# Optimization experiments

Measured on AMD Instinct MI355X. Metric: run time of the kernel, lower is better.

Reference implementation:

```python
import jax, jax.numpy as jnp
import numpy as np

WS = 11  # window_size
PAD = WS // 2
C1 = 0.01 ** 2
C2 = 0.03 ** 2

def _gaussian_window(ws=WS, sigma=1.5):
    # NOTE: original create_window hardcodes sigma=1.5 regardless of init arg
    x = np.arange(ws, dtype=np.float64)
    g = np.exp(-(x - ws // 2) ** 2 / (2.0 * sigma ** 2))
    g = g / g.sum()
    w = np.outer(g, g).astype(np.float32)
    return jnp.asarray(w)[None, None, :, :]  # [1,1,ws,ws] (OIHW)

def _conv(x, k):
    # x: [B,1,H,W], k: [1,1,ws,ws], SAME padding via explicit pad
    return jax.lax.conv_general_dilated(
        x, k, window_strides=(1, 1), padding=[(PAD, PAD), (PAD, PAD)],
        dimension_numbers=('NCHW', 'OIHW', 'NCHW'))

def setup_inputs() -> dict:
    key = jax.random.key(0)
    k1, k2 = jax.random.split(key)
    B, H, W = 32, 768, 768
    pred = jax.random.uniform(k1, (B, 1, H, W), dtype=jnp.float32)
    y = jax.random.uniform(k2, (B, 1, H, W), dtype=jnp.float32)
    return {"pred": pred, "y": y}

def reference(pred, y):
    k = _gaussian_window()
    mu1 = _conv(pred, k)
    mu2 = _conv(y, k)
    mu1_sq = mu1 * mu1
    mu2_sq = mu2 * mu2
    mu1_mu2 = mu1 * mu2
    sigma1_sq = _conv(pred * pred, k) - mu1_sq
    sigma2_sq = _conv(y * y, k) - mu2_sq
    sigma12 = _conv(pred * y, k) - mu1_mu2
    luminance = (2.0 * mu1_mu2 + C1) / (mu1_sq + mu2_sq + C1)
    contrast = (2.0 * sigma12 + C2) / (sigma1_sq + sigma2_sq + C2)
    structure = (sigma12 + C2 / 2.0) / (jnp.sqrt(sigma1_sq * sigma2_sq) + C2 / 2.0)
    ssim_map = luminance * contrast * structure  # [B,1,H,W]
    per_sample = jnp.mean(ssim_map, axis=(1, 2, 3))  # mean per sample, as in the loop
    return jnp.mean(per_sample)
```

## Files before the change

### kernel.cpp

```cpp
#include <hip/hip_runtime.h>

#define TW 32
#define TH 32
#define SH 42
#define HPITCH 36
#define BLOCK 256
#define IMG_W 768
#define IMG_H 768
#define IMG_B 32
#define GX_ (IMG_W / TW)
#define GY_ (IMG_H / TH)
#define NBLOCKS (GX_ * GY_ * IMG_B)

#define W0 0.00102838f
#define W1 0.00759876f
#define W2 0.03600077f
#define W3 0.10936069f
#define W4 0.21300554f
#define W5 0.26601173f

__global__ __launch_bounds__(BLOCK, 5) void ssim_tile_kernel(
    const float* __restrict__ pred, const float* __restrict__ yin,
    float* __restrict__ partial)
{
    constexpr float GW[11] = {W0, W1, W2, W3, W4, W5, W4, W3, W2, W1, W0};

    __shared__ __align__(16) float Hb[5][SH][HPITCH];
    __shared__ float wsum[BLOCK / 64];

    const int tid = threadIdx.x;
    const int x0 = blockIdx.x * TW;
    const int y0 = blockIdx.y * TH;
    const size_t base = (size_t)blockIdx.z * (size_t)(IMG_H * IMG_W);
    const float* pb = pred + base;
    const float* yb = yin + base;

    const bool interior = (x0 >= 8) && (x0 + TW + 8 <= IMG_W) &&
                          (y0 >= 5) && (y0 + TH + 5 <= IMG_H);

    for (int it = tid; it < SH * 8; it += BLOCK) {
        const int hr = it >> 3;
        const int c0 = (it & 7) << 2;
        const int gy = y0 + hr - 5;
        float p[14], q[14];

        if (interior) {
            const float* rp = pb + (size_t)gy * IMG_W + (x0 + c0 - 8);
            const float* rq = yb + (size_t)gy * IMG_W + (x0 + c0 - 8);
            p[0] = rp[3];
            *(float4*)(p + 1) = *(const float4*)(rp + 4);
            *(float4*)(p + 5) = *(const float4*)(rp + 8);
            *(float4*)(p + 9) = *(const float4*)(rp + 12);
            p[13] = rp[16];
            q[0] = rq[3];
            *(float4*)(q + 1) = *(const float4*)(rq + 4);
            *(float4*)(q + 5) = *(const float4*)(rq + 8);
            *(float4*)(q + 9) = *(const float4*)(rq + 12);
            q[13] = rq[16];
        } else {
            if (gy >= 0 && gy < IMG_H) {
                const float* rowp = pb + (size_t)gy * IMG_W;
                const float* rowq = yb + (size_t)gy * IMG_W;
                #pragma unroll
                for (int k = 0; k < 14; ++k) {
                    const int gx = x0 + c0 - 5 + k;
                    const bool in = (gx >= 0) && (gx < IMG_W);
                    p[k] = in ? rowp[gx] : 0.f;
                    q[k] = in ? rowq[gx] : 0.f;
                }
            } else {
                #pragma unroll
                for (int k = 0; k < 14; ++k) { p[k] = 0.f; q[k] = 0.f; }
            }
        }

        {
            float a0 = 0.f, a1 = 0.f, a2 = 0.f, a3 = 0.f;
            #pragma unroll
            for (int t = 0; t < 11; ++t) {
                const float w = GW[t];
                a0 += w * p[t]; a1 += w * p[t + 1];
                a2 += w * p[t + 2]; a3 += w * p[t + 3];
            }
            *(float4*)&Hb[0][hr][c0] = make_float4(a0, a1, a2, a3);
        }
        {
            float a0 = 0.f, a1 = 0.f, a2 = 0.f, a3 = 0.f;
            #pragma unroll
            for (int t = 0; t < 11; ++t) {
                const float w = GW[t];
                a0 += w * q[t]; a1 += w * q[t + 1];
                a2 += w * q[t + 2]; a3 += w * q[t + 3];
            }
            *(float4*)&Hb[1][hr][c0] = make_float4(a0, a1, a2, a3);
        }
        {
            float t14[14];
            #pragma unroll
            for (int k = 0; k < 14; ++k) t14[k] = p[k] * p[k];
            float a0 = 0.f, a1 = 0.f, a2 = 0.f, a3 = 0.f;
            #pragma unroll
            for (int t = 0; t < 11; ++t) {
                const float w = GW[t];
                a0 += w * t14[t]; a1 += w * t14[t + 1];
                a2 += w * t14[t + 2]; a3 += w * t14[t + 3];
            }
            *(float4*)&Hb[2][hr][c0] = make_float4(a0, a1, a2, a3);
        }
        {
            float t14[14];
            #pragma unroll
            for (int k = 0; k < 14; ++k) t14[k] = q[k] * q[k];
            float a0 = 0.f, a1 = 0.f, a2 = 0.f, a3 = 0.f;
            #pragma unroll
            for (int t = 0; t < 11; ++t) {
                const float w = GW[t];
                a0 += w * t14[t]; a1 += w * t14[t + 1];
                a2 += w * t14[t + 2]; a3 += w * t14[t + 3];
            }
            *(float4*)&Hb[3][hr][c0] = make_float4(a0, a1, a2, a3);
        }
        {
            float t14[14];
            #pragma unroll
            for (int k = 0; k < 14; ++k) t14[k] = p[k] * q[k];
            float a0 = 0.f, a1 = 0.f, a2 = 0.f, a3 = 0.f;
            #pragma unroll
            for (int t = 0; t < 11; ++t) {
                const float w = GW[t];
                a0 += w * t14[t]; a1 += w * t14[t + 1];
                a2 += w * t14[t + 2]; a3 += w * t14[t + 3];
            }
            *(float4*)&Hb[4][hr][c0] = make_float4(a0, a1, a2, a3);
        }
    }
    __syncthreads();

    const int vc  = tid & 31;
    const int vr0 = (tid >> 5) << 2;
    float acc[5][4];
    #pragma unroll
    for (int ch = 0; ch < 5; ++ch) {
        const float* hb = &Hb[ch][vr0][vc];
        float v[14];
        #pragma unroll
        for (int j = 0; j < 14; ++j) v[j] = hb[j * HPITCH];
        #pragma unroll
        for (int o = 0; o < 4; ++o) {
            float a = 0.f;
            #pragma unroll
            for (int t = 0; t < 11; ++t)
                a += GW[t] * v[o + t];
            acc[ch][o] = a;
        }
    }

    const float C1f = 1e-4f;
    const float C2f = 9e-4f;
    float lsum = 0.f;
    #pragma unroll
    for (int o = 0; o < 4; ++o) {
        float mu1 = acc[0][o], mu2 = acc[1][o];
        float m11 = acc[2][o], m22 = acc[3][o], m12 = acc[4][o];
        float mu1s = mu1 * mu1;
        float mu2s = mu2 * mu2;
        float mu12 = mu1 * mu2;
        float s1  = m11 - mu1s;
        float s2  = m22 - mu2s;
        float s12 = m12 - mu12;
        float num = (2.f * mu12 + C1f) * (2.f * s12 + C2f) * (s12 + 0.5f * C2f);
        float den = (mu1s + mu2s + C1f) * (s1 + s2 + C2f) * (sqrtf(s1 * s2) + 0.5f * C2f);
        lsum += num / den;
    }

    #pragma unroll
    for (int off = 32; off > 0; off >>= 1)
        lsum += __shfl_xor(lsum, off);
    const int wid  = tid >> 6;
    const int lane = tid & 63;
    if (lane == 0) wsum[wid] = lsum;
    __syncthreads();
    if (tid == 0) {
        const int bid = (blockIdx.z * GY_ + blockIdx.y) * GX_ + blockIdx.x;
        partial[bid] = wsum[0] + wsum[1] + wsum[2] + wsum[3];
    }
}

__global__ __launch_bounds__(1024) void ssim_reduce_kernel(
    const float* __restrict__ partial, float* __restrict__ out)
{
    __shared__ double sd[1024];
    double s = 0.0;
    const float4* p4 = (const float4*)partial;
    for (int i = threadIdx.x; i < NBLOCKS / 4; i += 1024) {
        float4 v = p4[i];
        s += (double)v.x + (double)v.y + (double)v.z + (double)v.w;
    }
    sd[threadIdx.x] = s;
    __syncthreads();
    #pragma unroll
    for (int st = 512; st > 0; st >>= 1) {
        if (threadIdx.x < st) sd[threadIdx.x] += sd[threadIdx.x + st];
        __syncthreads();
    }
    if (threadIdx.x == 0)
        out[0] = (float)(sd[0] * (1.0 / ((double)IMG_B * IMG_H * IMG_W)));
}

extern "C" void kernel_launch(void* const* d_in, const int* in_sizes, int n_in,
                              void* d_out, int out_size, void* d_ws, size_t ws_size,
                              hipStream_t stream)
{
    const float* pred = (const float*)d_in[0];
    const float* yin  = (const float*)d_in[1];
    float* out     = (float*)d_out;
    float* partial = (float*)d_ws;

    dim3 grid(GX_, GY_, IMG_B);
    ssim_tile_kernel<<<grid, BLOCK, 0, stream>>>(pred, yin, partial);
    ssim_reduce_kernel<<<1, 1024, 0, stream>>>(partial, out);
}
```

Before: 247.8 us.

## Split SSIM tile into two passes to shrink shared memory and raise occupancy

Splits the separable convolution into two passes. The first pass computes and vertically reduces the means using a two-channel buffer. The second pass reloads the inputs and computes the three second-moment channels in a three-channel shared buffer. This cuts shared memory per block from five channels to three, so launch bounds can rise from 5 to 8 blocks per CU. The cost is loading the input tile twice and an extra barrier. The change also swaps sqrtf and the division for hardware approximate sqrt and reciprocal, which may slightly change precision.

```diff
diff --git a/kernel.cpp b/kernel.cpp
--- a/kernel.cpp
+++ b/kernel.cpp
@@ -19,13 +19,26 @@
 #define W4 0.21300554f
 #define W5 0.26601173f
 
-__global__ __launch_bounds__(BLOCK, 5) void ssim_tile_kernel(
+__device__ __forceinline__ void hconv14(const float x[14], float* dst)
+{
+    constexpr float GW[11] = {W0, W1, W2, W3, W4, W5, W4, W3, W2, W1, W0};
+    float a0 = 0.f, a1 = 0.f, a2 = 0.f, a3 = 0.f;
+    #pragma unroll
+    for (int t = 0; t < 11; ++t) {
+        const float w = GW[t];
+        a0 += w * x[t];     a1 += w * x[t + 1];
+        a2 += w * x[t + 2]; a3 += w * x[t + 3];
+    }
+    *(float4*)dst = make_float4(a0, a1, a2, a3);
+}
+
+__global__ __launch_bounds__(BLOCK, 8) void ssim_tile_kernel(
     const float* __restrict__ pred, const float* __restrict__ yin,
     float* __restrict__ partial)
 {
     constexpr float GW[11] = {W0, W1, W2, W3, W4, W5, W4, W3, W2, W1, W0};
 
-    __shared__ __align__(16) float Hb[5][SH][HPITCH];
+    __shared__ __align__(16) float Hb[3][SH][HPITCH];
     __shared__ float wsum[BLOCK / 64];
 
     const int tid = threadIdx.x;
@@ -37,6 +50,9 @@
 
     const bool interior = (x0 >= 8) && (x0 + TW + 8 <= IMG_W) &&
                           (y0 >= 5) && (y0 + TH + 5 <= IMG_H);
+
+    const int vc  = tid & 31;
+    const int vr0 = (tid >> 5) << 2;
 
     for (int it = tid; it < SH * 8; it += BLOCK) {
         const int hr = it >> 3;
@@ -73,85 +89,102 @@
                 for (int k = 0; k < 14; ++k) { p[k] = 0.f; q[k] = 0.f; }
             }
         }
-
-        {
-            float a0 = 0.f, a1 = 0.f, a2 = 0.f, a3 = 0.f;
-            #pragma unroll
-            for (int t = 0; t < 11; ++t) {
-                const float w = GW[t];
-                a0 += w * p[t]; a1 += w * p[t + 1];
-                a2 += w * p[t + 2]; a3 += w * p[t + 3];
-            }
-            *(float4*)&Hb[0][hr][c0] = make_float4(a0, a1, a2, a3);
-        }
-        {
-            float a0 = 0.f, a1 = 0.f, a2 = 0.f, a3 = 0.f;
-            #pragma unroll
-            for (int t = 0; t < 11; ++t) {
-                const float w = GW[t];
-                a0 += w * q[t]; a1 += w * q[t + 1];
-                a2 += w * q[t + 2]; a3 += w * q[t + 3];
-            }
-            *(float4*)&Hb[1][hr][c0] = make_float4(a0, a1, a2, a3);
-        }
-        {
-            float t14[14];
-            #pragma unroll
-            for (int k = 0; k < 14; ++k) t14[k] = p[k] * p[k];
-            float a0 = 0.f, a1 = 0.f, a2 = 0.f, a3 = 0.f;
-            #pragma unroll
-            for (int t = 0; t < 11; ++t) {
-                const float w = GW[t];
-                a0 += w * t14[t]; a1 += w * t14[t + 1];
-                a2 += w * t14[t + 2]; a3 += w * t14[t + 3];
-            }
-            *(float4*)&Hb[2][hr][c0] = make_float4(a0, a1, a2, a3);
-        }
-        {
-            float t14[14];
-            #pragma unroll
-            for (int k = 0; k < 14; ++k) t14[k] = q[k] * q[k];
-            float a0 = 0.f, a1 = 0.f, a2 = 0.f, a3 = 0.f;
-            #pragma unroll
-            for (int t = 0; t < 11; ++t) {
-                const float w = GW[t];
-                a0 += w * t14[t]; a1 += w * t14[t + 1];
-                a2 += w * t14[t + 2]; a3 += w * t14[t + 3];
-            }
-            *(float4*)&Hb[3][hr][c0] = make_float4(a0, a1, a2, a3);
-        }
-        {
-            float t14[14];
-            #pragma unroll
-            for (int k = 0; k < 14; ++k) t14[k] = p[k] * q[k];
-            float a0 = 0.f, a1 = 0.f, a2 = 0.f, a3 = 0.f;
-            #pragma unroll
-            for (int t = 0; t < 11; ++t) {
-                const float w = GW[t];
-                a0 += w * t14[t]; a1 += w * t14[t + 1];
-                a2 += w * t14[t + 2]; a3 += w * t14[t + 3];
-            }
-            *(float4*)&Hb[4][hr][c0] = make_float4(a0, a1, a2, a3);
-        }
-    }
-    __syncthreads();
-
-    const int vc  = tid & 31;
-    const int vr0 = (tid >> 5) << 2;
-    float acc[5][4];
-    #pragma unroll
-    for (int ch = 0; ch < 5; ++ch) {
-        const float* hb = &Hb[ch][vr0][vc];
+        hconv14(p, &Hb[0][hr][c0]);
+        hconv14(q, &Hb[1][hr][c0]);
+    }
+    __syncthreads();
+
+    float mu1v[4], mu2v[4];
+    {
         float v[14];
-        #pragma unroll
-        for (int j = 0; j < 14; ++j) v[j] = hb[j * HPITCH];
+        const float* hb0 = &Hb[0][vr0][vc];
+        #pragma unroll
+        for (int j = 0; j < 14; ++j) v[j] = hb0[j * HPITCH];
         #pragma unroll
         for (int o = 0; o < 4; ++o) {
             float a = 0.f;
             #pragma unroll
-            for (int t = 0; t < 11; ++t)
-                a += GW[t] * v[o + t];
-            acc[ch][o] = a;
+            for (int t = 0; t < 11; ++t) a += GW[t] * v[o + t];
+            mu1v[o] = a;
+        }
+        const float* hb1 = &Hb[1][vr0][vc];
+        #pragma unroll
+        for (int j = 0; j < 14; ++j) v[j] = hb1[j * HPITCH];
+        #pragma unroll
+        for (int o = 0; o < 4; ++o) {
+            float a = 0.f;
+            #pragma unroll
+            for (int t = 0; t < 11; ++t) a += GW[t] * v[o + t];
+            mu2v[o] = a;
+        }
+    }
+    __syncthreads();
+
+    for (int it = tid; it < SH * 8; it += BLOCK) {
+        const int hr = it >> 3;
+        const int c0 = (it & 7) << 2;
+        const int gy = y0 + hr - 5;
+        float p[14], q[14];
+
+        if (interior) {
+            const float* rp = pb + (size_t)gy * IMG_W + (x0 + c0 - 8);
+            const float* rq = yb + (size_t)gy * IMG_W + (x0 + c0 - 8);
+            p[0] = rp[3];
+            *(float4*)(p + 1) = *(const float4*)(rp + 4);
+            *(float4*)(p + 5) = *(const float4*)(rp + 8);
+            *(float4*)(p + 9) = *(const float4*)(rp + 12);
+            p[13] = rp[16];
+            q[0] = rq[3];
+            *(float4*)(q + 1) = *(const float4*)(rq + 4);
+            *(float4*)(q + 5) = *(const float4*)(rq + 8);
+            *(float4*)(q + 9) = *(const float4*)(rq + 12);
+            q[13] = rq[16];
+        } else {
+            if (gy >= 0 && gy < IMG_H) {
+                const float* rowp = pb + (size_t)gy * IMG_W;
+                const float* rowq = yb + (size_t)gy * IMG_W;
+                #pragma unroll
+                for (int k = 0; k < 14; ++k) {
+                    const int gx = x0 + c0 - 5 + k;
+                    const bool in = (gx >= 0) && (gx < IMG_W);
+                    p[k] = in ? rowp[gx] : 0.f;
+                    q[k] = in ? rowq[gx] : 0.f;
+                }
+            } else {
+                #pragma unroll
+                for (int k = 0; k < 14; ++k) { p[k] = 0.f; q[k] = 0.f; }
+            }
+        }
+        float t14[14];
+        #pragma unroll
+        for (int k = 0; k < 14; ++k) t14[k] = p[k] * p[k];
+        hconv14(t14, &Hb[0][hr][c0]);
+        #pragma unroll
+        for (int k = 0; k < 14; ++k) t14[k] = q[k] * q[k];
+        hconv14(t14, &Hb[1][hr][c0]);
+        #pragma unroll
+        for (int k = 0; k < 14; ++k) t14[k] = p[k] * q[k];
+        hconv14(t14, &Hb[2][hr][c0]);
+    }
+    __syncthreads();
+
+    float m11v[4], m22v[4], m12v[4];
+    {
+        float v[14];
+        #pragma unroll
+        for (int ch = 0; ch < 3; ++ch) {
+            const float* hb = &Hb[ch][vr0][vc];
+            #pragma unroll
+            for (int j = 0; j < 14; ++j) v[j] = hb[j * HPITCH];
+            #pragma unroll
+            for (int o = 0; o < 4; ++o) {
+                float a = 0.f;
+                #pragma unroll
+                for (int t = 0; t < 11; ++t) a += GW[t] * v[o + t];
+                if (ch == 0) m11v[o] = a;
+                else if (ch == 1) m22v[o] = a;
+                else m12v[o] = a;
+            }
         }
     }
 
@@ -160,17 +193,17 @@
     float lsum = 0.f;
     #pragma unroll
     for (int o = 0; o < 4; ++o) {
-        float mu1 = acc[0][o], mu2 = acc[1][o];
-        float m11 = acc[2][o], m22 = acc[3][o], m12 = acc[4][o];
+        float mu1 = mu1v[o], mu2 = mu2v[o];
         float mu1s = mu1 * mu1;
         float mu2s = mu2 * mu2;
         float mu12 = mu1 * mu2;
-        float s1  = m11 - mu1s;
-        float s2  = m22 - mu2s;
-        float s12 = m12 - mu12;
+        float s1  = m11v[o] - mu1s;
+        float s2  = m22v[o] - mu2s;
+        float s12 = m12v[o] - mu12;
         float num = (2.f * mu12 + C1f) * (2.f * s12 + C2f) * (s12 + 0.5f * C2f);
-        float den = (mu1s + mu2s + C1f) * (s1 + s2 + C2f) * (sqrtf(s1 * s2) + 0.5f * C2f);
-        lsum += num / den;
+        float den = (mu1s + mu2s + C1f) * (s1 + s2 + C2f) *
+                    (__builtin_amdgcn_sqrtf(s1 * s2) + 0.5f * C2f);
+        lsum += num * __builtin_amdgcn_rcpf(den);
     }
 
     #pragma unroll
```

Result: slower. 464.9 us (+87.6%).

## Pack pred/y channel pairs into float2 to use packed FMA for Gaussian blur

Applied to the files above, without the earlier changes.

Interleaves the pred and y values (and their squares) into two-wide vectors so both horizontal and vertical 11-tap passes can use packed fp32 math (v_pk_fma) on paired channels. Shared memory is reorganized into two float2 planes plus one scalar plane for pred*y. The final SSIM division and sqrt are replaced with hardware approximate rcp and sqrt intrinsics. This aims to halve the FMA instruction count in the compute-bound blur, at the cost of slightly lower precision and possible LDS bank pattern changes from 8-byte elements.

```diff
diff --git a/kernel.cpp b/kernel.cpp
--- a/kernel.cpp
+++ b/kernel.cpp
@@ -1,8 +1,11 @@
 #include <hip/hip_runtime.h>
+
+typedef float f32x2 __attribute__((ext_vector_type(2)));
 
 #define TW 32
 #define TH 32
 #define SH 42
+#define PITCH2 34
 #define HPITCH 36
 #define BLOCK 256
 #define IMG_W 768
@@ -19,13 +22,17 @@
 #define W4 0.21300554f
 #define W5 0.26601173f
 
+__device__ __forceinline__ f32x2 sp2(float s) { f32x2 v; v.x = s; v.y = s; return v; }
+
 __global__ __launch_bounds__(BLOCK, 5) void ssim_tile_kernel(
     const float* __restrict__ pred, const float* __restrict__ yin,
     float* __restrict__ partial)
 {
     constexpr float GW[11] = {W0, W1, W2, W3, W4, W5, W4, W3, W2, W1, W0};
 
-    __shared__ __align__(16) float Hb[5][SH][HPITCH];
+    __shared__ __align__(16) f32x2 Hmu[SH][PITCH2];
+    __shared__ __align__(16) f32x2 Hsq[SH][PITCH2];
+    __shared__ __align__(16) float Hpq[SH][HPITCH];
     __shared__ float wsum[BLOCK / 64];
 
     const int tid = threadIdx.x;
@@ -74,85 +81,95 @@
             }
         }
 
+        f32x2 d[14];
+        #pragma unroll
+        for (int k = 0; k < 14; ++k) { f32x2 t; t.x = p[k]; t.y = q[k]; d[k] = t; }
+
+        {
+            f32x2 a0 = sp2(0.f), a1 = sp2(0.f), a2 = sp2(0.f), a3 = sp2(0.f);
+            #pragma unroll
+            for (int k = 0; k < 14; ++k) {
+                const f32x2 v = d[k];
+                if (k <= 10)           a0 += sp2(GW[k])     * v;
+                if (k >= 1 && k <= 11) a1 += sp2(GW[k - 1]) * v;
+                if (k >= 2 && k <= 12) a2 += sp2(GW[k - 2]) * v;
+                if (k >= 3)            a3 += sp2(GW[k - 3]) * v;
+            }
+            Hmu[hr][c0]     = a0;
+            Hmu[hr][c0 + 1] = a1;
+            Hmu[hr][c0 + 2] = a2;
+            Hmu[hr][c0 + 3] = a3;
+        }
+        {
+            f32x2 a0 = sp2(0.f), a1 = sp2(0.f), a2 = sp2(0.f), a3 = sp2(0.f);
+            #pragma unroll
+            for (int k = 0; k < 14; ++k) {
+                const f32x2 v = d[k] * d[k];
+                if (k <= 10)           a0 += sp2(GW[k])     * v;
+                if (k >= 1 && k <= 11) a1 += sp2(GW[k - 1]) * v;
+                if (k >= 2 && k <= 12) a2 += sp2(GW[k - 2]) * v;
+                if (k >= 3)            a3 += sp2(GW[k - 3]) * v;
+            }
+            Hsq[hr][c0]     = a0;
+            Hsq[hr][c0 + 1] = a1;
+            Hsq[hr][c0 + 2] = a2;
+            Hsq[hr][c0 + 3] = a3;
+        }
         {
             float a0 = 0.f, a1 = 0.f, a2 = 0.f, a3 = 0.f;
             #pragma unroll
-            for (int t = 0; t < 11; ++t) {
-                const float w = GW[t];
-                a0 += w * p[t]; a1 += w * p[t + 1];
-                a2 += w * p[t + 2]; a3 += w * p[t + 3];
-            }
-            *(float4*)&Hb[0][hr][c0] = make_float4(a0, a1, a2, a3);
-        }
-        {
-            float a0 = 0.f, a1 = 0.f, a2 = 0.f, a3 = 0.f;
-            #pragma unroll
-            for (int t = 0; t < 11; ++t) {
-                const float w = GW[t];
-                a0 += w * q[t]; a1 += w * q[t + 1];
-                a2 += w * q[t + 2]; a3 += w * q[t + 3];
-            }
-            *(float4*)&Hb[1][hr][c0] = make_float4(a0, a1, a2, a3);
-        }
-        {
-            float t14[14];
-            #pragma unroll
-            for (int k = 0; k < 14; ++k) t14[k] = p[k] * p[k];
-            float a0 = 0.f, a1 = 0.f, a2 = 0.f, a3 = 0.f;
-            #pragma unroll
-            for (int t = 0; t < 11; ++t) {
-                const float w = GW[t];
-                a0 += w * t14[t]; a1 += w * t14[t + 1];
-                a2 += w * t14[t + 2]; a3 += w * t14[t + 3];
-            }
-            *(float4*)&Hb[2][hr][c0] = make_float4(a0, a1, a2, a3);
-        }
-        {
-            float t14[14];
-            #pragma unroll
-            for (int k = 0; k < 14; ++k) t14[k] = q[k] * q[k];
-            float a0 = 0.f, a1 = 0.f, a2 = 0.f, a3 = 0.f;
-            #pragma unroll
-            for (int t = 0; t < 11; ++t) {
-                const float w = GW[t];
-                a0 += w * t14[t]; a1 += w * t14[t + 1];
-                a2 += w * t14[t + 2]; a3 += w * t14[t + 3];
-            }
-            *(float4*)&Hb[3][hr][c0] = make_float4(a0, a1, a2, a3);
-        }
-        {
-            float t14[14];
-            #pragma unroll
-            for (int k = 0; k < 14; ++k) t14[k] = p[k] * q[k];
-            float a0 = 0.f, a1 = 0.f, a2 = 0.f, a3 = 0.f;
-            #pragma unroll
-            for (int t = 0; t < 11; ++t) {
-                const float w = GW[t];
-                a0 += w * t14[t]; a1 += w * t14[t + 1];
-                a2 += w * t14[t + 2]; a3 += w * t14[t + 3];
-            }
-            *(float4*)&Hb[4][hr][c0] = make_float4(a0, a1, a2, a3);
+            for (int k = 0; k < 14; ++k) {
+                const float v = d[k].x * d[k].y;
+                if (k <= 10)           a0 += GW[k]     * v;
+                if (k >= 1 && k <= 11) a1 += GW[k - 1] * v;
+                if (k >= 2 && k <= 12) a2 += GW[k - 2] * v;
+                if (k >= 3)            a3 += GW[k - 3] * v;
+            }
+            *(float4*)&Hpq[hr][c0] = make_float4(a0, a1, a2, a3);
         }
     }
     __syncthreads();
 
     const int vc  = tid & 31;
     const int vr0 = (tid >> 5) << 2;
-    float acc[5][4];
-    #pragma unroll
-    for (int ch = 0; ch < 5; ++ch) {
-        const float* hb = &Hb[ch][vr0][vc];
-        float v[14];
-        #pragma unroll
-        for (int j = 0; j < 14; ++j) v[j] = hb[j * HPITCH];
-        #pragma unroll
-        for (int o = 0; o < 4; ++o) {
-            float a = 0.f;
-            #pragma unroll
-            for (int t = 0; t < 11; ++t)
-                a += GW[t] * v[o + t];
-            acc[ch][o] = a;
-        }
+
+    f32x2 MU0, MU1, MU2, MU3, SQ0, SQ1, SQ2, SQ3;
+    float PQ0, PQ1, PQ2, PQ3;
+    {
+        f32x2 a0 = sp2(0.f), a1 = sp2(0.f), a2 = sp2(0.f), a3 = sp2(0.f);
+        #pragma unroll
+        for (int k = 0; k < 14; ++k) {
+            const f32x2 v = Hmu[vr0 + k][vc];
+            if (k <= 10)           a0 += sp2(GW[k])     * v;
+            if (k >= 1 && k <= 11) a1 += sp2(GW[k - 1]) * v;
+            if (k >= 2 && k <= 12) a2 += sp2(GW[k - 2]) * v;
+            if (k >= 3)            a3 += sp2(GW[k - 3]) * v;
+        }
+        MU0 = a0; MU1 = a1; MU2 = a2; MU3 = a3;
+    }
+    {
+        f32x2 a0 = sp2(0.f), a1 = sp2(0.f), a2 = sp2(0.f), a3 = sp2(0.f);
+        #pragma unroll
+        for (int k = 0; k < 14; ++k) {
+            const f32x2 v = Hsq[vr0 + k][vc];
+            if (k <= 10)           a0 += sp2(GW[k])     * v;
+            if (k >= 1 && k <= 11) a1 += sp2(GW[k - 1]) * v;
+            if (k >= 2 && k <= 12) a2 += sp2(GW[k - 2]) * v;
+            if (k >= 3)            a3 += sp2(GW[k - 3]) * v;
+        }
+        SQ0 = a0; SQ1 = a1; SQ2 = a2; SQ3 = a3;
+    }
+    {
+        float a0 = 0.f, a1 = 0.f, a2 = 0.f, a3 = 0.f;
+        #pragma unroll
+        for (int k = 0; k < 14; ++k) {
+            const float v = Hpq[vr0 + k][vc];
+            if (k <= 10)           a0 += GW[k]     * v;
+            if (k >= 1 && k <= 11) a1 += GW[k - 1] * v;
+            if (k >= 2 && k <= 12) a2 += GW[k - 2] * v;
+            if (k >= 3)            a3 += GW[k - 3] * v;
+        }
+        PQ0 = a0; PQ1 = a1; PQ2 = a2; PQ3 = a3;
     }
 
     const float C1f = 1e-4f;
@@ -160,17 +177,17 @@
     float lsum = 0.f;
     #pragma unroll
     for (int o = 0; o < 4; ++o) {
-        float mu1 = acc[0][o], mu2 = acc[1][o];
-        float m11 = acc[2][o], m22 = acc[3][o], m12 = acc[4][o];
-        float mu1s = mu1 * mu1;
-        float mu2s = mu2 * mu2;
-        float mu12 = mu1 * mu2;
-        float s1  = m11 - mu1s;
-        float s2  = m22 - mu2s;
-        float s12 = m12 - mu12;
-        float num = (2.f * mu12 + C1f) * (2.f * s12 + C2f) * (s12 + 0.5f * C2f);
-        float den = (mu1s + mu2s + C1f) * (s1 + s2 + C2f) * (sqrtf(s1 * s2) + 0.5f * C2f);
-        lsum += num / den;
+        const f32x2 mu = (o == 0) ? MU0 : (o == 1) ? MU1 : (o == 2) ? MU2 : MU3;
+        const f32x2 sq = (o == 0) ? SQ0 : (o == 1) ? SQ1 : (o == 2) ? SQ2 : SQ3;
+        const float pq = (o == 0) ? PQ0 : (o == 1) ? PQ1 : (o == 2) ? PQ2 : PQ3;
+        const f32x2 musq = mu * mu;
+        const float mu12 = mu.x * mu.y;
+        const f32x2 sig  = sq - musq;
+        const float s12  = pq - mu12;
+        const float num = (2.f * mu12 + C1f) * (2.f * s12 + C2f) * (s12 + 0.5f * C2f);
+        const float den = (musq.x + musq.y + C1f) * (sig.x + sig.y + C2f) *
+                          (__builtin_amdgcn_sqrtf(sig.x * sig.y) + 0.5f * C2f);
+        lsum += num * __builtin_amdgcn_rcpf(den);
     }
 
     #pragma unroll
```

New measurement: 230.5 us. 1.07x faster.
